# Kernel optimization log

Measured on AMD Instinct MI355X. Metric: run time of the kernel, lower is better.

Reference implementation:

```python
import jax, jax.numpy as jnp
import numpy as np

N = 100000      # num nodes
E = 800000      # num edges
IN = 256        # in_features
D = 64          # out_features per head
H = 4           # num_heads
EF = 64         # edge_feats
NET = 8         # num_etype
SLOPE = 0.2     # leaky relu negative slope


def setup_inputs() -> dict:
    key = jax.random.key(0)
    ks = jax.random.split(key, 12)
    s = 0.05
    h = jax.random.normal(ks[0], (N, IN), jnp.float32)
    row = jax.random.randint(ks[1], (E,), 0, N, dtype=jnp.int32)   # src
    col = jax.random.randint(ks[2], (E,), 0, N, dtype=jnp.int32)   # dst
    tp = jax.random.randint(ks[3], (E,), 0, NET, dtype=jnp.int32)  # edge type
    W = jax.random.normal(ks[4], (IN, D * H), jnp.float32) * s
    W_e = jax.random.normal(ks[5], (EF, EF * H), jnp.float32) * s
    edge_emb = jax.random.normal(ks[6], (NET, EF), jnp.float32) * s
    a_l = jax.random.normal(ks[7], (1, H, D), jnp.float32) * s
    a_r = jax.random.normal(ks[8], (1, H, D), jnp.float32) * s
    a_e = jax.random.normal(ks[9], (1, H, EF), jnp.float32) * s
    res_W = jax.random.normal(ks[10], (IN, D * H), jnp.float32) * s
    res_b = jnp.zeros((D * H,), jnp.float32)
    return {"h": h, "W": W, "W_e": W_e, "edge_emb": edge_emb,
            "a_l": a_l, "a_r": a_r, "a_e": a_e,
            "res_W": res_W, "res_b": res_b,
            "row": row, "col": col, "tp": tp}


def reference(h, W, W_e, edge_emb, a_l, a_r, a_e, res_W, res_b, row, col, tp):
    # node projection -> [N, H, D]; nan-guard as in the original
    emb = jnp.nan_to_num((h @ W).reshape(-1, H, D), nan=0.0)
    # edge-type embedding projection -> [NET, H, EF]
    e = (edge_emb @ W_e).reshape(-1, H, EF)
    # per-edge attention logits [E, H]
    h_l = (a_l * emb).sum(-1)[row]
    h_r = (a_r * emb).sum(-1)[col]
    h_e = (a_e * e).sum(-1)[tp]
    att = jax.nn.leaky_relu(h_l + h_r + h_e, SLOPE)
    # segment softmax over edges grouped by destination node
    m = jax.ops.segment_max(att, col, num_segments=N)          # [N, H]
    ex = jnp.exp(att - m[col])                                 # [E, H]
    denom = jax.ops.segment_sum(ex, col, num_segments=N)      # [N, H]
    alpha = ex / denom[col]                                    # [E, H]
    # gather-multiply-scatter message passing: [E, H, D] -> [N, H, D]
    msg = emb[row] * alpha[:, :, None]
    out = jax.ops.segment_sum(msg, col, num_segments=N).reshape(N, H * D)
    # residual linear + elu activation
    out = out + h @ res_W + res_b
    return jax.nn.elu(out)
```

## Files before the change

kernel.cpp:

```cpp
#include <hip/hip_runtime.h>

#define N_NODES 100000
#define E_EDGES 800000
#define IN_F 256
#define D_HEAD 64
#define H_HEADS 4
#define EF_F 64
#define NET_T 8
#define HD 256
#define SLOPE 0.2f
#define NTILES ((N_NODES + 63) / 64)
#define NGROUP ((NTILES + 7) / 8)
#define EPT 8
#define HBLOCKS ((E_EDGES + 256 * EPT - 1) / (256 * EPT))

typedef unsigned short u16;
typedef unsigned long long u64;
typedef __attribute__((ext_vector_type(8))) short bf16x8;
typedef __attribute__((ext_vector_type(4))) float f32x4;

static __device__ __forceinline__ u16 f2bf(float f) {
    unsigned int u = __float_as_uint(f);
    unsigned int r = u + 0x7FFFu + ((u >> 16) & 1u);
    return (u16)(r >> 16);
}
static __device__ __forceinline__ float bf2f(unsigned int u) {
    return __uint_as_float(u << 16);
}

__global__ void k_pre(const float* __restrict__ W, const float* __restrict__ resW,
                      u16* __restrict__ Bfrag,
                      const float* __restrict__ edge_emb, const float* __restrict__ W_e,
                      const float* __restrict__ a_e, float* __restrict__ s_e) {
    const int b = blockIdx.x;
    const int tid = threadIdx.x;
    if (b < 64) {
        const int gid = b * 256 + tid;
        const int lane = gid & 63;
        const int fragid = gid >> 6;
        const int n = fragid & 3;
        const int ks = (fragid >> 2) & 7;
        const int g = fragid >> 5;
        const int c = g * 64 + n * 16 + (lane & 15);
        const int k0 = ks * 32 + (lane >> 4) * 8;
        const float* src = (c < HD) ? &W[c] : &resW[c - HD];
        u16 tmp[8];
#pragma unroll
        for (int j = 0; j < 8; ++j)
            tmp[j] = f2bf(src[(size_t)(k0 + j) * HD]);
        *reinterpret_cast<uint4*>(&Bfrag[(size_t)fragid * 512 + lane * 8]) =
            *reinterpret_cast<const uint4*>(tmp);
    } else {
        const int t  = tid >> 5;
        const int h  = (tid >> 3) & 3;
        const int fc = tid & 7;
        float part = 0.f;
        for (int j = 0; j < 8; ++j) {
            const int f = fc * 8 + j;
            float acc = 0.f;
            for (int k = 0; k < EF_F; ++k)
                acc += edge_emb[t * EF_F + k] * W_e[k * (EF_F * H_HEADS) + h * EF_F + f];
            part += a_e[h * EF_F + f] * acc;
        }
        for (int off = 1; off < 8; off <<= 1)
            part += __shfl_xor(part, off, 64);
        if (fc == 0) s_e[t * H_HEADS + h] = part;
    }
}

__global__ void k_hist(const int* __restrict__ col, int* __restrict__ counts) {
    const int base = (blockIdx.x * 256 + threadIdx.x) * EPT;
    if (base + EPT <= E_EDGES) {
        const int4 c0 = *reinterpret_cast<const int4*>(&col[base]);
        const int4 c1 = *reinterpret_cast<const int4*>(&col[base + 4]);
        atomicAdd(&counts[c0.x], 1);
        atomicAdd(&counts[c0.y], 1);
        atomicAdd(&counts[c0.z], 1);
        atomicAdd(&counts[c0.w], 1);
        atomicAdd(&counts[c1.x], 1);
        atomicAdd(&counts[c1.y], 1);
        atomicAdd(&counts[c1.z], 1);
        atomicAdd(&counts[c1.w], 1);
    } else {
        for (int e = base; e < E_EDGES; ++e)
            atomicAdd(&counts[col[e]], 1);
    }
}

__global__ __launch_bounds__(256, 3)
void k_mfma(const float* __restrict__ A, const u16* __restrict__ Bfrag,
            const float* __restrict__ a_l, const float* __restrict__ a_r,
            const float* __restrict__ resb,
            u16* __restrict__ emb_bf, float* __restrict__ s_l, float* __restrict__ s_r,
            u16* __restrict__ res_bf) {
    __shared__ char At[32768];
    const int tid = threadIdx.x;
    const int lane = tid & 63;
    const int wv = tid >> 6;
    const int gidx = blockIdx.x >> 4;
    const int x = blockIdx.x & 15;
    const int tile = gidx * 8 + (x & 7);
    if (tile >= NTILES) return;
    const int by = x >> 3;
    const int wid = (by << 2) | wv;
    const int row0 = tile * 64;

#pragma unroll
    for (int half = 0; half < 2; ++half) {
        float4 v[8];
#pragma unroll
        for (int c = 0; c < 8; ++c) {
            const int lin8 = (half * 8 + c) * 2048 + tid * 8;
            const int r_lin = lin8 >> 9;
            int grow = row0 + r_lin;
            if (grow >= N_NODES) grow = N_NODES - 1;
            const int colb = lin8 & 511;
            v[c] = *reinterpret_cast<const float4*>(&A[(size_t)grow * IN_F + (colb >> 1)]);
        }
#pragma unroll
        for (int c = 0; c < 8; ++c) {
            const int lin8 = (half * 8 + c) * 2048 + tid * 8;
            const int r_lin = lin8 >> 9;
            uint2 o;
            o.x = (unsigned)f2bf(v[c].x) | ((unsigned)f2bf(v[c].y) << 16);
            o.y = (unsigned)f2bf(v[c].z) | ((unsigned)f2bf(v[c].w) << 16);
            *reinterpret_cast<uint2*>(&At[lin8 ^ ((r_lin & 7) << 4)]) = o;
        }
    }
    __syncthreads();

    const int lr = lane & 15;
    const int lg = lane >> 4;
    const int xr = (lr & 7) << 4;
    const int klg = lg * 16;

    int rowbase[4];
#pragma unroll
    for (int m = 0; m < 4; ++m) rowbase[m] = (m * 16 + lr) * 512;

    const u16* bp = Bfrag + (size_t)wid * 16384 + lane * 8;

    f32x4 acc[4][4] = {};
#pragma unroll
    for (int ks = 0; ks < 8; ++ks) {
        bf16x8 af[4], bfr[4];
        const int kx = ((ks << 6) + klg) ^ xr;
#pragma unroll
        for (int n = 0; n < 4; ++n)
            bfr[n] = *reinterpret_cast<const bf16x8*>(&bp[ks * 2048 + n * 512]);
#pragma unroll
        for (int m = 0; m < 4; ++m)
            af[m] = *reinterpret_cast<const bf16x8*>(&At[rowbase[m] + kx]);
#pragma unroll
        for (int m = 0; m < 4; ++m)
#pragma unroll
            for (int n = 0; n < 4; ++n)
                acc[m][n] = __builtin_amdgcn_mfma_f32_16x16x32_bf16(bfr[n], af[m], acc[m][n], 0, 0, 0);
    }

    if (by == 0) {
        const int h = wv;
        float4 alv[4], arv[4];
#pragma unroll
        for (int n = 0; n < 4; ++n) {
            alv[n] = *reinterpret_cast<const float4*>(&a_l[h * D_HEAD + n * 16 + lg * 4]);
            arv[n] = *reinterpret_cast<const float4*>(&a_r[h * D_HEAD + n * 16 + lg * 4]);
        }
#pragma unroll
        for (int m = 0; m < 4; ++m) {
            const int node = row0 + m * 16 + lr;
            float dl = 0.f, dr = 0.f;
            u64 pk[4];
#pragma unroll
            for (int n = 0; n < 4; ++n) {
                float v0 = acc[m][n][0], v1 = acc[m][n][1], v2 = acc[m][n][2], v3 = acc[m][n][3];
                v0 = isnan(v0) ? 0.f : v0;
                v1 = isnan(v1) ? 0.f : v1;
                v2 = isnan(v2) ? 0.f : v2;
                v3 = isnan(v3) ? 0.f : v3;
                dl += v0 * alv[n].x + v1 * alv[n].y + v2 * alv[n].z + v3 * alv[n].w;
                dr += v0 * arv[n].x + v1 * arv[n].y + v2 * arv[n].z + v3 * arv[n].w;
                pk[n] = (u64)f2bf(v0) | ((u64)f2bf(v1) << 16) |
                        ((u64)f2bf(v2) << 32) | ((u64)f2bf(v3) << 48);
            }
            if (node < N_NODES) {
                const size_t base = (size_t)node * HD + h * D_HEAD + lg * 4;
#pragma unroll
                for (int n = 0; n < 4; ++n)
                    *reinterpret_cast<u64*>(&emb_bf[base + n * 16]) = pk[n];
            }
            dl += __shfl_xor(dl, 16, 64); dr += __shfl_xor(dr, 16, 64);
            dl += __shfl_xor(dl, 32, 64); dr += __shfl_xor(dr, 32, 64);
            if (lg == 0 && node < N_NODES) {
                s_l[node * H_HEADS + h] = dl;
                s_r[node * H_HEADS + h] = dr;
            }
        }
    } else {
        const int c0 = wv * 64 + lg * 4;
        float4 rb[4];
#pragma unroll
        for (int n = 0; n < 4; ++n)
            rb[n] = *reinterpret_cast<const float4*>(&resb[c0 + n * 16]);
#pragma unroll
        for (int m = 0; m < 4; ++m) {
            const int node = row0 + m * 16 + lr;
            if (node < N_NODES) {
                const size_t base = (size_t)node * HD + c0;
#pragma unroll
                for (int n = 0; n < 4; ++n) {
                    const float v0 = acc[m][n][0] + rb[n].x;
                    const float v1 = acc[m][n][1] + rb[n].y;
                    const float v2 = acc[m][n][2] + rb[n].z;
                    const float v3 = acc[m][n][3] + rb[n].w;
                    const u64 pk = (u64)f2bf(v0) | ((u64)f2bf(v1) << 16) |
                                   ((u64)f2bf(v2) << 32) | ((u64)f2bf(v3) << 48);
                    *reinterpret_cast<u64*>(&res_bf[base + n * 16]) = pk;
                }
            }
        }
    }
}

__global__ void k_scan1(const int* __restrict__ counts, int* __restrict__ row_ptr,
                        int* __restrict__ partials) {
    __shared__ int sd[256];
    const int t = threadIdx.x, b = blockIdx.x;
    const int base = b * 1024 + t * 4;
    int v[4];
#pragma unroll
    for (int j = 0; j < 4; ++j) v[j] = (base + j < N_NODES) ? counts[base + j] : 0;
    const int s = v[0] + v[1] + v[2] + v[3];
    sd[t] = s;
    __syncthreads();
    for (int off = 1; off < 256; off <<= 1) {
        int y = (t >= off) ? sd[t - off] : 0;
        __syncthreads();
        sd[t] += y;
        __syncthreads();
    }
    int p = sd[t] - s;
#pragma unroll
    for (int j = 0; j < 4; ++j) {
        if (base + j < N_NODES) row_ptr[base + j] = p;
        p += v[j];
    }
    if (t == 255) partials[b] = sd[255];
}

__global__ void k_scan2(int* __restrict__ partials) {
    __shared__ int sd[128];
    const int t = threadIdx.x;
    const int v = (t < 98) ? partials[t] : 0;
    sd[t] = v;
    __syncthreads();
    for (int off = 1; off < 128; off <<= 1) {
        int y = (t >= off) ? sd[t - off] : 0;
        __syncthreads();
        sd[t] += y;
        __syncthreads();
    }
    if (t < 98) partials[t] = sd[t] - v;
}

__global__ void k_scan3(int* __restrict__ row_ptr, int* __restrict__ fill,
                        const int* __restrict__ partials) {
    const int i = blockIdx.x * 256 + threadIdx.x;
    if (i < N_NODES) {
        const int v = row_ptr[i] + partials[i >> 10];
        row_ptr[i] = v;
        fill[i] = v;
    }
    if (i == 0) row_ptr[N_NODES] = E_EDGES;
}

__global__ void k_scatter(const int* __restrict__ row, const int* __restrict__ col,
                          const int* __restrict__ tp, int* __restrict__ fill,
                          int* __restrict__ perm_rt) {
    const int base = (blockIdx.x * 256 + threadIdx.x) * EPT;
    if (base + EPT <= E_EDGES) {
        const int4 r0 = *reinterpret_cast<const int4*>(&row[base]);
        const int4 r1 = *reinterpret_cast<const int4*>(&row[base + 4]);
        const int4 c0 = *reinterpret_cast<const int4*>(&col[base]);
        const int4 c1 = *reinterpret_cast<const int4*>(&col[base + 4]);
        const int4 t0 = *reinterpret_cast<const int4*>(&tp[base]);
        const int4 t1 = *reinterpret_cast<const int4*>(&tp[base + 4]);
        int p[8];
        p[0] = atomicAdd(&fill[c0.x], 1);
        p[1] = atomicAdd(&fill[c0.y], 1);
        p[2] = atomicAdd(&fill[c0.z], 1);
        p[3] = atomicAdd(&fill[c0.w], 1);
        p[4] = atomicAdd(&fill[c1.x], 1);
        p[5] = atomicAdd(&fill[c1.y], 1);
        p[6] = atomicAdd(&fill[c1.z], 1);
        p[7] = atomicAdd(&fill[c1.w], 1);
        perm_rt[p[0]] = r0.x | (t0.x << 20);
        perm_rt[p[1]] = r0.y | (t0.y << 20);
        perm_rt[p[2]] = r0.z | (t0.z << 20);
        perm_rt[p[3]] = r0.w | (t0.w << 20);
        perm_rt[p[4]] = r1.x | (t1.x << 20);
        perm_rt[p[5]] = r1.y | (t1.y << 20);
        perm_rt[p[6]] = r1.z | (t1.z << 20);
        perm_rt[p[7]] = r1.w | (t1.w << 20);
    } else {
        for (int e = base; e < E_EDGES; ++e) {
            const int p = atomicAdd(&fill[col[e]], 1);
            perm_rt[p] = row[e] | (tp[e] << 20);
        }
    }
}

__global__ __launch_bounds__(256)
void k_aggregate(const int* __restrict__ row_ptr, const int* __restrict__ perm_rt,
                 const float* __restrict__ s_l, const float* __restrict__ s_r,
                 const float* __restrict__ s_e,
                 const u16* __restrict__ emb_bf, const u16* __restrict__ res_bf,
                 float* __restrict__ outp) {
    const int wave = threadIdx.x >> 6;
    const int lane = threadIdx.x & 63;
    const int n = blockIdx.x * 4 + wave;
    const int h = lane >> 4;
    const int start = row_ptr[n], end = row_ptr[n + 1];
    const size_t o = (size_t)n * HD + lane * 4;
    const u64 rv = *reinterpret_cast<const u64*>(&res_bf[o]);
    const float srh = s_r[n * H_HEADS + h];

    float a0 = 0.f, a1 = 0.f, a2 = 0.f, a3 = 0.f, den = 0.f;
    for (int i = start; i < end; i += 8) {
        int r[8], t[8]; float sl[8]; u64 ev[8];
#pragma unroll
        for (int j = 0; j < 8; ++j) {
            const int idx = (i + j < end) ? (i + j) : (end - 1);
            const int q = perm_rt[idx];
            r[j] = q & 0xFFFFF;
            t[j] = q >> 20;
        }
#pragma unroll
        for (int j = 0; j < 8; ++j)
            sl[j] = s_l[r[j] * H_HEADS + h];
#pragma unroll
        for (int j = 0; j < 8; ++j)
            ev[j] = *reinterpret_cast<const u64*>(&emb_bf[(size_t)r[j] * HD + lane * 4]);
#pragma unroll
        for (int j = 0; j < 8; ++j) {
            float lg = sl[j] + srh + s_e[t[j] * H_HEADS + h];
            lg = (lg > 0.f) ? lg : SLOPE * lg;
            float ex = __expf(lg);
            ex = (i + j < end) ? ex : 0.f;
            const unsigned lo = (unsigned)ev[j], hi = (unsigned)(ev[j] >> 32);
            a0 += ex * __uint_as_float(lo << 16);
            a1 += ex * __uint_as_float(lo & 0xFFFF0000u);
            a2 += ex * __uint_as_float(hi << 16);
            a3 += ex * __uint_as_float(hi & 0xFFFF0000u);
            den += ex;
        }
    }
    const float inv = (den > 0.f) ? 1.f / den : 0.f;
    f32x4 out;
    float x;
    x = a0 * inv + bf2f((unsigned)(rv) & 0xFFFFu);       out.x = (x > 0.f) ? x : __expf(x) - 1.f;
    x = a1 * inv + bf2f((unsigned)(rv >> 16) & 0xFFFFu); out.y = (x > 0.f) ? x : __expf(x) - 1.f;
    x = a2 * inv + bf2f((unsigned)(rv >> 32) & 0xFFFFu); out.z = (x > 0.f) ? x : __expf(x) - 1.f;
    x = a3 * inv + bf2f((unsigned)(rv >> 48) & 0xFFFFu); out.w = (x > 0.f) ? x : __expf(x) - 1.f;
    __builtin_nontemporal_store(out, reinterpret_cast<f32x4*>(&outp[o]));
}

extern "C" void kernel_launch(void* const* d_in, const int* in_sizes, int n_in,
                              void* d_out, int out_size, void* d_ws, size_t ws_size,
                              hipStream_t stream) {
    const float* h    = (const float*)d_in[0];
    const float* W    = (const float*)d_in[1];
    const float* W_e  = (const float*)d_in[2];
    const float* eemb = (const float*)d_in[3];
    const float* a_l  = (const float*)d_in[4];
    const float* a_r  = (const float*)d_in[5];
    const float* a_e  = (const float*)d_in[6];
    const float* resW = (const float*)d_in[7];
    const float* resb = (const float*)d_in[8];
    const int* row = (const int*)d_in[9];
    const int* col = (const int*)d_in[10];
    const int* tp  = (const int*)d_in[11];
    float* outp = (float*)d_out;

    char* ws = (char*)d_ws;
    size_t off = 0;
    auto alloc = [&](size_t b) { size_t o = off; off += (b + 255) & ~(size_t)255; return o; };
    u16*  Bfrag   = (u16*)(ws + alloc((size_t)512 * IN_F * 2));
    u16*  emb_bf  = (u16*)(ws + alloc((size_t)N_NODES * HD * 2));
    u16*  res_bf  = (u16*)(ws + alloc((size_t)N_NODES * HD * 2));
    float* s_l    = (float*)(ws + alloc((size_t)N_NODES * H_HEADS * 4));
    float* s_r    = (float*)(ws + alloc((size_t)N_NODES * H_HEADS * 4));
    float* s_e    = (float*)(ws + alloc(NET_T * H_HEADS * 4));
    int*  counts  = (int*)(ws + alloc((size_t)N_NODES * 4));
    int*  row_ptr = (int*)(ws + alloc((size_t)(N_NODES + 1) * 4));
    int*  fill    = (int*)(ws + alloc((size_t)N_NODES * 4));
    int*  perm_rt = (int*)(ws + alloc((size_t)E_EDGES * 4));
    int*  partials= (int*)(ws + alloc(128 * 4));

    (void)hipMemsetAsync(counts, 0, (size_t)N_NODES * 4, stream);
    k_pre<<<65, 256, 0, stream>>>(W, resW, Bfrag, eemb, W_e, a_e, s_e);
    k_hist<<<HBLOCKS, 256, 0, stream>>>(col, counts);
    k_mfma<<<NGROUP * 16, 256, 0, stream>>>(h, Bfrag, a_l, a_r, resb, emb_bf, s_l, s_r, res_bf);
    k_scan1<<<98, 256, 0, stream>>>(counts, row_ptr, partials);
    k_scan2<<<1, 128, 0, stream>>>(partials);
    k_scan3<<<(N_NODES + 255) / 256, 256, 0, stream>>>(row_ptr, fill, partials);
    k_scatter<<<HBLOCKS, 256, 0, stream>>>(row, col, tp, fill, perm_rt);
    k_aggregate<<<N_NODES / 4, 256, 0, stream>>>(row_ptr, perm_rt, s_l, s_r, s_e,
                                                 emb_bf, res_bf, outp);
}
```

Measured before the change: 290.2 us.

## Fuse CSR build into one cooperative kernel with grid syncs; zero counts in k_pre

The histogram, three-stage scan and scatter kernels are merged into a single cooperative kernel of 391 blocks that separates the phases with grid-wide syncs. The memset of the counts array moves into extra blocks of the preprocessing kernel. The aim is to cut several kernel launches and inter-kernel gaps in the CSR construction. The cost is the grid.sync barriers and the requirement that all blocks be co-resident. The scan phase still relies on the block count covering the 98 scan blocks and the 100000 fill indices.

```diff
diff --git a/kernel.cpp b/kernel.cpp
--- a/kernel.cpp
+++ b/kernel.cpp
@@ -1,4 +1,5 @@
 #include <hip/hip_runtime.h>
+#include <hip/hip_cooperative_groups.h>
 
 #define N_NODES 100000
 #define E_EDGES 800000
@@ -12,7 +13,7 @@
 #define NTILES ((N_NODES + 63) / 64)
 #define NGROUP ((NTILES + 7) / 8)
 #define EPT 8
-#define HBLOCKS ((E_EDGES + 256 * EPT - 1) / (256 * EPT))
+#define CSRBLOCKS ((E_EDGES + 256 * EPT - 1) / (256 * EPT))
 
 typedef unsigned short u16;
 typedef unsigned long long u64;
@@ -31,7 +32,8 @@
 __global__ void k_pre(const float* __restrict__ W, const float* __restrict__ resW,
                       u16* __restrict__ Bfrag,
                       const float* __restrict__ edge_emb, const float* __restrict__ W_e,
-                      const float* __restrict__ a_e, float* __restrict__ s_e) {
+                      const float* __restrict__ a_e, float* __restrict__ s_e,
+                      int* __restrict__ counts) {
     const int b = blockIdx.x;
     const int tid = threadIdx.x;
     if (b < 64) {
@@ -50,7 +52,7 @@
             tmp[j] = f2bf(src[(size_t)(k0 + j) * HD]);
         *reinterpret_cast<uint4*>(&Bfrag[(size_t)fragid * 512 + lane * 8]) =
             *reinterpret_cast<const uint4*>(tmp);
-    } else {
+    } else if (b == 64) {
         const int t  = tid >> 5;
         const int h  = (tid >> 3) & 3;
         const int fc = tid & 7;
@@ -65,25 +67,129 @@
         for (int off = 1; off < 8; off <<= 1)
             part += __shfl_xor(part, off, 64);
         if (fc == 0) s_e[t * H_HEADS + h] = part;
-    }
-}
-
-__global__ void k_hist(const int* __restrict__ col, int* __restrict__ counts) {
-    const int base = (blockIdx.x * 256 + threadIdx.x) * EPT;
-    if (base + EPT <= E_EDGES) {
-        const int4 c0 = *reinterpret_cast<const int4*>(&col[base]);
-        const int4 c1 = *reinterpret_cast<const int4*>(&col[base + 4]);
-        atomicAdd(&counts[c0.x], 1);
-        atomicAdd(&counts[c0.y], 1);
-        atomicAdd(&counts[c0.z], 1);
-        atomicAdd(&counts[c0.w], 1);
-        atomicAdd(&counts[c1.x], 1);
-        atomicAdd(&counts[c1.y], 1);
-        atomicAdd(&counts[c1.z], 1);
-        atomicAdd(&counts[c1.w], 1);
     } else {
-        for (int e = base; e < E_EDGES; ++e)
-            atomicAdd(&counts[col[e]], 1);
+        const int base = (b - 65) * 1024 + tid * 4;
+#pragma unroll
+        for (int j = 0; j < 4; ++j)
+            if (base + j < N_NODES) counts[base + j] = 0;
+    }
+}
+
+__global__ void k_csr(const int* __restrict__ row, const int* __restrict__ col,
+                      const int* __restrict__ tp,
+                      int* __restrict__ counts, int* __restrict__ row_ptr,
+                      int* __restrict__ fill, int* __restrict__ partials,
+                      int* __restrict__ perm_rt) {
+    cooperative_groups::grid_group grid = cooperative_groups::this_grid();
+    __shared__ int sd[256];
+    const int b = blockIdx.x;
+    const int t = threadIdx.x;
+
+    {
+        const int base = (b * 256 + t) * EPT;
+        if (base + EPT <= E_EDGES) {
+            const int4 c0 = *reinterpret_cast<const int4*>(&col[base]);
+            const int4 c1 = *reinterpret_cast<const int4*>(&col[base + 4]);
+            atomicAdd(&counts[c0.x], 1);
+            atomicAdd(&counts[c0.y], 1);
+            atomicAdd(&counts[c0.z], 1);
+            atomicAdd(&counts[c0.w], 1);
+            atomicAdd(&counts[c1.x], 1);
+            atomicAdd(&counts[c1.y], 1);
+            atomicAdd(&counts[c1.z], 1);
+            atomicAdd(&counts[c1.w], 1);
+        } else {
+            for (int e = base; e < E_EDGES; ++e)
+                atomicAdd(&counts[col[e]], 1);
+        }
+    }
+    grid.sync();
+
+    if (b < 98) {
+        const int base = b * 1024 + t * 4;
+        int v[4];
+#pragma unroll
+        for (int j = 0; j < 4; ++j) v[j] = (base + j < N_NODES) ? counts[base + j] : 0;
+        const int s = v[0] + v[1] + v[2] + v[3];
+        sd[t] = s;
+        __syncthreads();
+        for (int off = 1; off < 256; off <<= 1) {
+            int y = (t >= off) ? sd[t - off] : 0;
+            __syncthreads();
+            sd[t] += y;
+            __syncthreads();
+        }
+        int p = sd[t] - s;
+#pragma unroll
+        for (int j = 0; j < 4; ++j) {
+            if (base + j < N_NODES) row_ptr[base + j] = p;
+            p += v[j];
+        }
+        if (t == 255) partials[b] = sd[255];
+    }
+    grid.sync();
+
+    if (b == 0) {
+        int v = 0;
+        if (t < 128) {
+            v = (t < 98) ? partials[t] : 0;
+            sd[t] = v;
+        }
+        __syncthreads();
+        for (int off = 1; off < 128; off <<= 1) {
+            int y = 0;
+            if (t < 128 && t >= off) y = sd[t - off];
+            __syncthreads();
+            if (t < 128) sd[t] += y;
+            __syncthreads();
+        }
+        if (t < 98) partials[t] = sd[t] - v;
+    }
+    grid.sync();
+
+    {
+        const int i = b * 256 + t;
+        if (i < N_NODES) {
+            const int v = row_ptr[i] + partials[i >> 10];
+            row_ptr[i] = v;
+            fill[i] = v;
+        }
+        if (i == 0) row_ptr[N_NODES] = E_EDGES;
+    }
+    grid.sync();
+
+    {
+        const int base = (b * 256 + t) * EPT;
+        if (base + EPT <= E_EDGES) {
+            const int4 r0 = *reinterpret_cast<const int4*>(&row[base]);
+            const int4 r1 = *reinterpret_cast<const int4*>(&row[base + 4]);
+            const int4 c0 = *reinterpret_cast<const int4*>(&col[base]);
+            const int4 c1 = *reinterpret_cast<const int4*>(&col[base + 4]);
+            const int4 t0 = *reinterpret_cast<const int4*>(&tp[base]);
+            const int4 t1 = *reinterpret_cast<const int4*>(&tp[base + 4]);
+            int p[8];
+            p[0] = atomicAdd(&fill[c0.x], 1);
+            p[1] = atomicAdd(&fill[c0.y], 1);
+            p[2] = atomicAdd(&fill[c0.z], 1);
+            p[3] = atomicAdd(&fill[c0.w], 1);
+            p[4] = atomicAdd(&fill[c1.x], 1);
+            p[5] = atomicAdd(&fill[c1.y], 1);
+            p[6] = atomicAdd(&fill[c1.z], 1);
+            p[7] = atomicAdd(&fill[c1.w], 1);
+            perm_rt[p[0]] = r0.x | (t0.x << 20);
+            perm_rt[p[1]] = r0.y | (t0.y << 20);
+            perm_rt[p[2]] = r0.z | (t0.z << 20);
+            perm_rt[p[3]] = r0.w | (t0.w << 20);
+            perm_rt[p[4]] = r1.x | (t1.x << 20);
+            perm_rt[p[5]] = r1.y | (t1.y << 20);
+            perm_rt[p[6]] = r1.z | (t1.z << 20);
+            perm_rt[p[7]] = r1.w | (t1.w << 20);
+        } else {
+            for (int e = base; e < E_EDGES; ++e) {
+                const int p = atomicAdd(&fill[col[e]], 1);
+                perm_rt[p] = row[e] | (tp[e] << 20);
+            }
+        }
     }
 }
 
@@ -222,94 +328,6 @@
     }
 }
 
-__global__ void k_scan1(const int* __restrict__ counts, int* __restrict__ row_ptr,
-                        int* __restrict__ partials) {
-    __shared__ int sd[256];
-    const int t = threadIdx.x, b = blockIdx.x;
-    const int base = b * 1024 + t * 4;
-    int v[4];
-#pragma unroll
-    for (int j = 0; j < 4; ++j) v[j] = (base + j < N_NODES) ? counts[base + j] : 0;
-    const int s = v[0] + v[1] + v[2] + v[3];
-    sd[t] = s;
-    __syncthreads();
-    for (int off = 1; off < 256; off <<= 1) {
-        int y = (t >= off) ? sd[t - off] : 0;
-        __syncthreads();
-        sd[t] += y;
-        __syncthreads();
-    }
-    int p = sd[t] - s;
-#pragma unroll
-    for (int j = 0; j < 4; ++j) {
-        if (base + j < N_NODES) row_ptr[base + j] = p;
-        p += v[j];
-    }
-    if (t == 255) partials[b] = sd[255];
-}
-
-__global__ void k_scan2(int* __restrict__ partials) {
-    __shared__ int sd[128];
-    const int t = threadIdx.x;
-    const int v = (t < 98) ? partials[t] : 0;
-    sd[t] = v;
-    __syncthreads();
-    for (int off = 1; off < 128; off <<= 1) {
-        int y = (t >= off) ? sd[t - off] : 0;
-        __syncthreads();
-        sd[t] += y;
-        __syncthreads();
-    }
-    if (t < 98) partials[t] = sd[t] - v;
-}
-
-__global__ void k_scan3(int* __restrict__ row_ptr, int* __restrict__ fill,
-                        const int* __restrict__ partials) {
-    const int i = blockIdx.x * 256 + threadIdx.x;
-    if (i < N_NODES) {
-        const int v = row_ptr[i] + partials[i >> 10];
-        row_ptr[i] = v;
-        fill[i] = v;
-    }
-    if (i == 0) row_ptr[N_NODES] = E_EDGES;
-}
-
-__global__ void k_scatter(const int* __restrict__ row, const int* __restrict__ col,
-                          const int* __restrict__ tp, int* __restrict__ fill,
-                          int* __restrict__ perm_rt) {
-    const int base = (blockIdx.x * 256 + threadIdx.x) * EPT;
-    if (base + EPT <= E_EDGES) {
-        const int4 r0 = *reinterpret_cast<const int4*>(&row[base]);
-        const int4 r1 = *reinterpret_cast<const int4*>(&row[base + 4]);
-        const int4 c0 = *reinterpret_cast<const int4*>(&col[base]);
-        const int4 c1 = *reinterpret_cast<const int4*>(&col[base + 4]);
-        const int4 t0 = *reinterpret_cast<const int4*>(&tp[base]);
-        const int4 t1 = *reinterpret_cast<const int4*>(&tp[base + 4]);
-        int p[8];
-        p[0] = atomicAdd(&fill[c0.x], 1);
-        p[1] = atomicAdd(&fill[c0.y], 1);
-        p[2] = atomicAdd(&fill[c0.z], 1);
-        p[3] = atomicAdd(&fill[c0.w], 1);
-        p[4] = atomicAdd(&fill[c1.x], 1);
-        p[5] = atomicAdd(&fill[c1.y], 1);
-        p[6] = atomicAdd(&fill[c1.z], 1);
-        p[7] = atomicAdd(&fill[c1.w], 1);
-        perm_rt[p[0]] = r0.x | (t0.x << 20);
-        perm_rt[p[1]] = r0.y | (t0.y << 20);
-        perm_rt[p[2]] = r0.z | (t0.z << 20);
-        perm_rt[p[3]] = r0.w | (t0.w << 20);
-        perm_rt[p[4]] = r1.x | (t1.x << 20);
-        perm_rt[p[5]] = r1.y | (t1.y << 20);
-        perm_rt[p[6]] = r1.z | (t1.z << 20);
-        perm_rt[p[7]] = r1.w | (t1.w << 20);
-    } else {
-        for (int e = base; e < E_EDGES; ++e) {
-            const int p = atomicAdd(&fill[col[e]], 1);
-            perm_rt[p] = row[e] | (tp[e] << 20);
-        }
-    }
-}
-
 __global__ __launch_bounds__(256)
 void k_aggregate(const int* __restrict__ row_ptr, const int* __restrict__ perm_rt,
                  const float* __restrict__ s_l, const float* __restrict__ s_r,
@@ -397,14 +415,12 @@
     int*  perm_rt = (int*)(ws + alloc((size_t)E_EDGES * 4));
     int*  partials= (int*)(ws + alloc(128 * 4));
 
-    (void)hipMemsetAsync(counts, 0, (size_t)N_NODES * 4, stream);
-    k_pre<<<65, 256, 0, stream>>>(W, resW, Bfrag, eemb, W_e, a_e, s_e);
-    k_hist<<<HBLOCKS, 256, 0, stream>>>(col, counts);
+    k_pre<<<163, 256, 0, stream>>>(W, resW, Bfrag, eemb, W_e, a_e, s_e, counts);
+    void* csr_args[] = {(void*)&row, (void*)&col, (void*)&tp, (void*)&counts,
+                        (void*)&row_ptr, (void*)&fill, (void*)&partials, (void*)&perm_rt};
+    (void)hipLaunchCooperativeKernel((const void*)k_csr, dim3(CSRBLOCKS), dim3(256),
+                                     csr_args, 0, stream);
     k_mfma<<<NGROUP * 16, 256, 0, stream>>>(h, Bfrag, a_l, a_r, resb, emb_bf, s_l, s_r, res_bf);
-    k_scan1<<<98, 256, 0, stream>>>(counts, row_ptr, partials);
-    k_scan2<<<1, 128, 0, stream>>>(partials);
-    k_scan3<<<(N_NODES + 255) / 256, 256, 0, stream>>>(row_ptr, fill, partials);
-    k_scatter<<<HBLOCKS, 256, 0, stream>>>(row, col, tp, fill, perm_rt);
     k_aggregate<<<N_NODES / 4, 256, 0, stream>>>(row_ptr, perm_rt, s_l, s_r, s_e,
                                                  emb_bf, res_bf, outp);
 }
```

After: 458.7 us. 58.0% more time.
